# Kernel tuning notes

Hardware: AMD Instinct MI355X
Metric: run time of the kernel (lower is better)

The kernel has to match this reference:

```python
import jax, jax.numpy as jnp
import numpy as np

B, S, D, H = 2, 2048, 768, 12
HD = D // H  # head_dim = 64


def setup_inputs() -> dict:
    key = jax.random.key(0)
    ks = jax.random.split(key, 9)
    s = 1.0 / np.sqrt(D)
    return {
        "x": jax.random.normal(ks[0], (B, S, D), dtype=jnp.float32),
        "Wq": jax.random.normal(ks[1], (D, D), dtype=jnp.float32) * s,
        "bq": jnp.zeros((D,), dtype=jnp.float32),
        "Wk": jax.random.normal(ks[2], (D, D), dtype=jnp.float32) * s,
        "bk": jnp.zeros((D,), dtype=jnp.float32),
        "Wv": jax.random.normal(ks[3], (D, D), dtype=jnp.float32) * s,
        "bv": jnp.zeros((D,), dtype=jnp.float32),
        "Wo": jax.random.normal(ks[4], (D, D), dtype=jnp.float32) * s,
        "bo": jnpp if False else jnp.zeros((D,), dtype=jnp.float32),
    }


def reference(x, Wq, bq, Wk, bk, Wv, bv, Wo, bo):
    b, s, d = x.shape
    # projections, split heads: [b, h, s, hd]
    def proj(W, bias):
        y = x @ W + bias
        return y.reshape(b, s, H, HD).transpose(0, 2, 1, 3)

    q = proj(Wq, bq)
    k = proj(Wk, bk)
    v = proj(Wv, bv)

    scale = 1.0 / jnp.sqrt(jnp.float32(HD))
    scores = jnp.einsum("bhqd,bhkd->bhqk", q, k) * scale
    causal = jnp.tril(jnp.ones((s, s), dtype=bool))  # True where allowed
    scores = jnp.where(causal, scores, -jnp.inf)
    attn = jax.nn.softmax(scores, axis=-1)
    ctx = jnp.einsum("bhqk,bhkd->bhqd", attn, v)
    ctx = ctx.transpose(0, 2, 1, 3).reshape(b, s, d)
    return ctx @ Wo + bo
```

## Files before the change

### kernel.cpp

```cpp
#include <hip/hip_runtime.h>
#include <stdint.h>

typedef unsigned short u16;
typedef __attribute__((ext_vector_type(8))) short s16x8;
typedef __attribute__((ext_vector_type(4))) float f32x4;
typedef __attribute__((ext_vector_type(16))) float f32x16;

#define MFMA_BF16(a, b, c) __builtin_amdgcn_mfma_f32_16x16x32_bf16((a), (b), (c), 0, 0, 0)
#define MFMA32(a, b, c) __builtin_amdgcn_mfma_f32_32x32x16_bf16((a), (b), (c), 0, 0, 0)

typedef const __attribute__((address_space(1))) uint32_t* gas1_t;
typedef __attribute__((address_space(3))) uint32_t* las3_t;
#define GLDS16(dst, src) __builtin_amdgcn_global_load_lds((gas1_t)(src), (las3_t)(dst), 16, 0, 0)

static __device__ __forceinline__ u16 f2bf(float f) {
    uint32_t u = __float_as_uint(f);
    u = (u + 0x7fffu + ((u >> 16) & 1u)) >> 16;
    return (u16)u;
}
static __device__ __forceinline__ uint32_t pk2bf(float a, float b) {
    return (uint32_t)f2bf(a) | ((uint32_t)f2bf(b) << 16);
}
static __device__ __forceinline__ float bf2f(u16 h) {
    return __uint_as_float(((uint32_t)h) << 16);
}

__global__ __launch_bounds__(256) void k_prep(const float* __restrict__ x, u16* __restrict__ xb,
                                              const float* __restrict__ w0, const float* __restrict__ w1,
                                              const float* __restrict__ w2, const float* __restrict__ w3,
                                              u16* __restrict__ t0, u16* __restrict__ t1,
                                              u16* __restrict__ t2, u16* __restrict__ t3) {
    __shared__ float tile[32][33];
    const int bid = blockIdx.x, t = threadIdx.x;
    if (bid < 1536) {
        const int i = (bid * 256 + t) * 8;
        f32x4 a = *(const f32x4*)(x + i);
        f32x4 b = *(const f32x4*)(x + i + 4);
        s16x8 r;
        r[0] = (short)f2bf(a[0]); r[1] = (short)f2bf(a[1]);
        r[2] = (short)f2bf(a[2]); r[3] = (short)f2bf(a[3]);
        r[4] = (short)f2bf(b[0]); r[5] = (short)f2bf(b[1]);
        r[6] = (short)f2bf(b[2]); r[7] = (short)f2bf(b[3]);
        *(s16x8*)(xb + i) = r;
        return;
    }
    const int u = bid - 1536;
    const int z = u / 576, r2 = u - z * 576;
    const float* W; u16* T;
    switch (z) {
        case 0:  W = w0; T = t0; break;
        case 1:  W = w1; T = t1; break;
        case 2:  W = w2; T = t2; break;
        default: W = w3; T = t3; break;
    }
    const int n0 = (r2 % 24) * 32, k0 = (r2 / 24) * 32;
    const int tx = t & 31, ty = t >> 5;
#pragma unroll
    for (int i = 0; i < 4; ++i)
        tile[ty + 8 * i][tx] = W[(size_t)(k0 + ty + 8 * i) * 768 + n0 + tx];
    __syncthreads();
#pragma unroll
    for (int i = 0; i < 4; ++i)
        T[(size_t)(n0 + ty + 8 * i) * 768 + k0 + tx] = f2bf(tile[tx][ty + 8 * i]);
}

__global__ __launch_bounds__(256) void k_gemm_qkv(
        const u16* __restrict__ A,
        const u16* __restrict__ btq, const u16* __restrict__ btk, const u16* __restrict__ btv,
        const float* __restrict__ bq, const float* __restrict__ bk, const float* __restrict__ bv,
        u16* __restrict__ outq, u16* __restrict__ outk, u16* __restrict__ outv) {
    __shared__ u16 lA[2][128 * 64];
    __shared__ u16 lB[2][64 * 64];
    const int cid = blockIdx.x;
    const int swz = (cid & 7) * 144 + (cid >> 3);
    const int sx = swz % 36, by = swz / 36;
    const int sel = sx / 12, nb = sx - sel * 12;
    const u16* Bt; const float* bias;
    if (sel == 0)      { Bt = btq; bias = bq; }
    else if (sel == 1) { Bt = btk; bias = bk; }
    else               { Bt = btv; bias = bv; }
    const int t = threadIdx.x, lane = t & 63, w = t >> 6;
    const int wr = w >> 1, wc = w & 1;
    const int c = lane & 15, g = lane >> 4;
    const int m0 = by * 128, n0 = nb * 64;
    f32x4 acc[4][2] = {};
    const int lr = lane >> 3, lg = lane & 7;
    const int swz8 = 8 * (lg ^ lr);
    const u16* gA = A  + (size_t)(m0 + w * 8 + lr) * 768 + swz8;
    const u16* gB = Bt + (size_t)(n0 + w * 8 + lr) * 768 + swz8;
#define STG_QKV(bb, kb)                                                        \
    {                                                                          \
        _Pragma("unroll")                                                      \
        for (int j = 0; j < 4; ++j)                                            \
            GLDS16(&lA[bb][j * 2048 + w * 512], gA + (size_t)j * 32 * 768 + (kb)); \
        _Pragma("unroll")                                                      \
        for (int j = 0; j < 2; ++j)                                            \
            GLDS16(&lB[bb][j * 2048 + w * 512], gB + (size_t)j * 32 * 768 + (kb)); \
    }
    STG_QKV(0, 0);
    for (int ki = 0; ki < 12; ++ki) {
        const int cur = ki & 1;
        if (ki + 1 < 12) {
            STG_QKV(cur ^ 1, (ki + 1) * 64);
            asm volatile("s_waitcnt vmcnt(6)" ::: "memory");
        } else {
            asm volatile("s_waitcnt vmcnt(0)" ::: "memory");
        }
        __builtin_amdgcn_sched_barrier(0);
        __builtin_amdgcn_s_barrier();
#pragma unroll
        for (int kh = 0; kh < 2; ++kh) {
            s16x8 af[4], bfr[2];
            const int gg = kh * 4 + g;
#pragma unroll
            for (int i = 0; i < 4; ++i) {
                const int ra = wr * 64 + i * 16 + c;
                af[i] = *(const s16x8*)&lA[cur][ra * 64 + 8 * (gg ^ (ra & 7))];
            }
#pragma unroll
            for (int j = 0; j < 2; ++j) {
                const int rb = wc * 32 + j * 16 + c;
                bfr[j] = *(const s16x8*)&lB[cur][rb * 64 + 8 * (gg ^ (rb & 7))];
            }
#pragma unroll
            for (int i = 0; i < 4; ++i)
#pragma unroll
                for (int j = 0; j < 2; ++j)
                    acc[i][j] = MFMA_BF16(af[i], bfr[j], acc[i][j]);
        }
        __builtin_amdgcn_s_barrier();
    }
#undef STG_QKV
    const float C2 = 0.18033688011112042f;
    const int h = nb;
    if (sel < 2) {
        u16* outp = (sel == 0) ? outq : outk;
        const float osc = (sel == 0) ? C2 : 1.0f;
#pragma unroll
        for (int i = 0; i < 4; ++i)
#pragma unroll
            for (int j = 0; j < 2; ++j) {
                const int hd = wc * 32 + j * 16 + c;
                const float bvv = bias[n0 + hd];
#pragma unroll
                for (int rr = 0; rr < 4; ++rr) {
                    const int m = m0 + wr * 64 + i * 16 + g * 4 + rr;
                    const int b = m >> 11, s = m & 2047;
                    outp[(((size_t)(b * 12 + h) * 2048 + s) << 6) + hd] =
                        f2bf((acc[i][j][rr] + bvv) * osc);
                }
            }
    } else {
#pragma unroll
        for (int i = 0; i < 4; ++i)
#pragma unroll
            for (int j = 0; j < 2; ++j) {
                const int hd = wc * 32 + j * 16 + c;
                const float bvv = bias[n0 + hd];
                const int m = m0 + wr * 64 + i * 16 + g * 4;
                const int b = m >> 11, s = m & 2047;
                uint64_t pk = (uint64_t)pk2bf(acc[i][j][0] + bvv, acc[i][j][1] + bvv) |
                              ((uint64_t)pk2bf(acc[i][j][2] + bvv, acc[i][j][3] + bvv) << 32);
                *(uint64_t*)&outv[((size_t)(b * 12 + h) * 64 + hd) * 2048 + s] = pk;
            }
    }
}

__global__ __launch_bounds__(256) void k_gemm_out(const u16* __restrict__ A,
                                                  const u16* __restrict__ Bt,
                                                  const float* __restrict__ bias,
                                                  float* __restrict__ out) {
    __shared__ u16 lA[2][64 * 64];
    __shared__ u16 lB[2][64 * 64];
    const int cid = blockIdx.x;
    const int swz = (cid & 7) * 96 + (cid >> 3);
    const int bx = swz % 12, by = swz / 12;
    const int t = threadIdx.x;
    const int lane = t & 63, w = t >> 6;
    const int wr = w >> 1, wc = w & 1;
    const int c = lane & 15, g = lane >> 4;
    const int m0 = by * 64, n0 = bx * 64;
    f32x4 acc[2][2] = {};
    const int lr = lane >> 3, lq = lane & 7;
    const int sq = (lq ^ lr) * 8;
    const u16* gA0 = A  + (size_t)(m0 + w * 16 + lr) * 768 + sq;
    const u16* gA1 = gA0 + 8 * 768;
    const u16* gB0 = Bt + (size_t)(n0 + w * 16 + lr) * 768 + sq;
    const u16* gB1 = gB0 + 8 * 768;
#define STG_OUT(bb, kb)                                                        \
    {                                                                          \
        GLDS16(&lA[bb][w * 1024], gA0 + (kb));                                 \
        GLDS16(&lA[bb][w * 1024 + 512], gA1 + (kb));                           \
        GLDS16(&lB[bb][w * 1024], gB0 + (kb));                                 \
        GLDS16(&lB[bb][w * 1024 + 512], gB1 + (kb));                           \
    }
    STG_OUT(0, 0);
    for (int ki = 0; ki < 12; ++ki) {
        const int cur = ki & 1;
        if (ki + 1 < 12) {
            STG_OUT(cur ^ 1, (ki + 1) * 64);
            asm volatile("s_waitcnt vmcnt(4)" ::: "memory");
        } else {
            asm volatile("s_waitcnt vmcnt(0)" ::: "memory");
        }
        __builtin_amdgcn_sched_barrier(0);
        __builtin_amdgcn_s_barrier();
#pragma unroll
        for (int st = 0; st < 2; ++st) {
            s16x8 af[2], bf[2];
            const int col = st * 32 + g * 8;
#pragma unroll
            for (int i = 0; i < 2; ++i) {
                int ra = wr * 32 + i * 16 + c;
                af[i] = *(const s16x8*)&lA[cur][ra * 64 + (col ^ ((ra & 7) << 3))];
                int rb = wc * 32 + i * 16 + c;
                bf[i] = *(const s16x8*)&lB[cur][rb * 64 + (col ^ ((rb & 7) << 3))];
            }
#pragma unroll
            for (int i = 0; i < 2; ++i)
#pragma unroll
                for (int j = 0; j < 2; ++j)
                    acc[i][j] = MFMA_BF16(af[i], bf[j], acc[i][j]);
        }
        __builtin_amdgcn_s_barrier();
    }
#undef STG_OUT
#pragma unroll
    for (int i = 0; i < 2; ++i)
#pragma unroll
        for (int j = 0; j < 2; ++j) {
            const int n = n0 + wc * 32 + j * 16 + c;
            const float bvv = bias[n];
#pragma unroll
            for (int rr = 0; rr < 4; ++rr) {
                const int m = m0 + wr * 32 + i * 16 + g * 4 + rr;
                out[(size_t)m * 768 + n] = acc[i][j][rr] + bvv;
            }
        }
}

__device__ static const signed char SLOT_QT[40] = {
    15,15,15,15, 14,14,14,14, 13,13,13,13, 12,12,12,12,
    11,11,11, 10,10,10, 9,9,9, 8,8,8, 7,7, 6,6, 5,5, 4,4, 3, 2, 1, 0};
__device__ static const signed char SLOT_SEG[40] = {
    0,1,2,3, 0,1,2,3, 0,1,2,3, 0,1,2,3,
    0,1,2, 0,1,2, 0,1,2, 0,1,2, 0,1, 0,1, 0,1, 0,1, 0, 0, 0, 0};

__global__ __launch_bounds__(256) void k_attn(const u16* __restrict__ qw,
                                              const u16* __restrict__ kw,
                                              const u16* __restrict__ vt,
                                              u16* __restrict__ ctxb,
                                              u16* __restrict__ pctx,
                                              float* __restrict__ pm,
                                              float* __restrict__ ps) {
    const int bid = blockIdx.x;
    const int slot = bid / 24, j24 = bid - slot * 24;
    const int bh = (j24 & 7) * 3 + (j24 >> 3);
    const int qt = SLOT_QT[slot], seg = SLOT_SEG[slot];
    const int nseg = (2 * (qt + 1) + 7) >> 3;
    const int ch0 = seg * 8;
    const int rem = 2 * (qt + 1) - ch0;
    const int nch = rem < 8 ? rem : 8;
    const int t = threadIdx.x, lane = t & 63, w = t >> 6;
    const int l31 = lane & 31, hi = lane >> 5;
    const int q0w = qt * 128 + w * 32;
    const u16* qp = qw + (size_t)bh * 2048 * 64;
    const u16* kp = kw + (size_t)bh * 2048 * 64;
    const u16* vp = vt + (size_t)bh * 64 * 2048;
    s16x8 qf[4];
#pragma unroll
    for (int dk = 0; dk < 4; ++dk)
        qf[dk] = *(const s16x8*)&qp[(size_t)(q0w + l31) * 64 + dk * 16 + hi * 8];
    const int lastq = q0w + 31;
    const int lastch = (lastq >> 6) + 1 - ch0;
    const int mynch = nch < lastch ? nch : lastch;
    f32x16 ct[2] = {};
    float m2 = -1e30f, ssum = 0.0f;
    for (int ci = 0; ci < mynch; ++ci) {
        const int Kc = (ch0 + ci) * 64;
        const u16* kr0 = kp + (size_t)(Kc + l31) * 64;
        const u16* kr1 = kp + (size_t)(Kc + 32 + l31) * 64;
        f32x16 st[2] = {};
#pragma unroll
        for (int dk = 0; dk < 4; ++dk) {
            const int gr = dk * 2 + hi;
            s16x8 kf0 = *(const s16x8*)&kr0[gr * 8];
            s16x8 kf1 = *(const s16x8*)&kr1[gr * 8];
            st[0] = MFMA32(kf0, qf[dk], st[0]);
            st[1] = MFMA32(kf1, qf[dk], st[1]);
        }
        const int qg = q0w + l31;
        float tv[32];
        if (Kc + 63 <= q0w) {
#pragma unroll
            for (int j = 0; j < 16; ++j) { tv[j] = st[0][j]; tv[16 + j] = st[1][j]; }
        } else {
            const int kb = Kc + 4 * hi;
#pragma unroll
            for (int j = 0; j < 16; ++j) {
                const int kloc = (j & 3) + 8 * (j >> 2);
                tv[j]      = (kb + kloc      <= qg) ? st[0][j] : -1e30f;
                tv[16 + j] = (kb + kloc + 32 <= qg) ? st[1][j] : -1e30f;
            }
        }
        float x16[16], x8[8], x4[4];
#pragma unroll
        for (int j = 0; j < 16; ++j) x16[j] = fmaxf(tv[j], tv[j + 16]);
#pragma unroll
        for (int j = 0; j < 8; ++j) x8[j] = fmaxf(x16[j], x16[j + 8]);
#pragma unroll
        for (int j = 0; j < 4; ++j) x4[j] = fmaxf(x8[j], x8[j + 4]);
        const float mt = fmaxf(fmaxf(x4[0], x4[1]), fmaxf(x4[2], x4[3]));
        if (!__all(mt <= m2 + 8.0f)) {
            float mq = fmaxf(mt, __shfl_xor(mt, 32));
            const float mnew = fmaxf(m2, mq);
            const float fac = __builtin_amdgcn_exp2f(m2 - mnew);
            ssum *= fac;
#pragma unroll
            for (int j = 0; j < 16; ++j) { ct[0][j] *= fac; ct[1][j] *= fac; }
            m2 = mnew;
        }
        float p[32];
#pragma unroll
        for (int j = 0; j < 32; ++j) p[j] = __builtin_amdgcn_exp2f(tv[j] - m2);
        float y16[16], y8[8], y4[4];
#pragma unroll
        for (int j = 0; j < 16; ++j) y16[j] = p[j] + p[j + 16];
#pragma unroll
        for (int j = 0; j < 8; ++j) y8[j] = y16[j] + y16[j + 8];
#pragma unroll
        for (int j = 0; j < 4; ++j) y4[j] = y8[j] + y8[j + 4];
        ssum += (y4[0] + y4[1]) + (y4[2] + y4[3]);
#pragma unroll
        for (int kt = 0; kt < 2; ++kt) {
            uint32_t pcv[8];
#pragma unroll
            for (int x = 0; x < 8; ++x) {
                const int j = kt * 16 + 4 * (x >> 1) + 2 * (x & 1);
                asm volatile("v_cvt_pk_bf16_f32 %0, %1, %2"
                             : "=v"(pcv[x]) : "v"(p[j]), "v"(p[j + 1]));
            }
#pragma unroll
            for (int kl = 0; kl < 2; ++kl) {
                uint32_t a0 = pcv[4 * kl],     b0 = pcv[4 * kl + 2];
                uint32_t a1 = pcv[4 * kl + 1], b1 = pcv[4 * kl + 3];
                asm volatile("v_permlane32_swap_b32 %0, %1" : "+v"(a0), "+v"(b0));
                asm volatile("v_permlane32_swap_b32 %0, %1" : "+v"(a1), "+v"(b1));
                union { uint32_t u[4]; s16x8 v; } pf;
                pf.u[0] = a0; pf.u[1] = a1; pf.u[2] = b0; pf.u[3] = b1;
                const int ko = Kc + (kt * 2 + kl) * 16 + hi * 8;
                s16x8 vf0 = *(const s16x8*)&vp[(size_t)l31 * 2048 + ko];
                s16x8 vf1 = *(const s16x8*)&vp[(size_t)(32 + l31) * 2048 + ko];
                ct[0] = MFMA32(vf0, pf.v, ct[0]);
                ct[1] = MFMA32(vf1, pf.v, ct[1]);
            }
        }
    }
    if (nseg == 1) {
        ssum += __shfl_xor(ssum, 32);
        const float inv = 1.0f / ssum;
        const int b = bh / 12, h = bh - b * 12;
        const size_t base = (size_t)(b * 2048 + q0w + l31) * 768 + h * 64;
#pragma unroll
        for (int ht = 0; ht < 2; ++ht)
#pragma unroll
            for (int a = 0; a < 4; ++a) {
                const int hd = ht * 32 + 8 * a + 4 * hi;
                uint64_t pk = (uint64_t)pk2bf(ct[ht][4 * a] * inv, ct[ht][4 * a + 1] * inv) |
                              ((uint64_t)pk2bf(ct[ht][4 * a + 2] * inv, ct[ht][4 * a + 3] * inv) << 32);
                *(uint64_t*)&ctxb[base + hd] = pk;
            }
    } else {
        const float srow = ssum + __shfl_xor(ssum, 32);
        const int ti = (bh * 16 + qt) * 4 + seg;
        const int row = w * 32 + l31;
        u16* pp = &pctx[(size_t)ti * 8192 + row * 64];
#pragma unroll
        for (int ht = 0; ht < 2; ++ht)
#pragma unroll
            for (int a = 0; a < 4; ++a) {
                const int hd = ht * 32 + 8 * a + 4 * hi;
                uint64_t pk = (uint64_t)pk2bf(ct[ht][4 * a], ct[ht][4 * a + 1]) |
                              ((uint64_t)pk2bf(ct[ht][4 * a + 2], ct[ht][4 * a + 3]) << 32);
                *(uint64_t*)&pp[hd] = pk;
            }
        if (hi == 0) {
            pm[ti * 128 + row] = m2;
            ps[ti * 128 + row] = srow;
        }
    }
}

__global__ __launch_bounds__(256) void k_attn_combine(const u16* __restrict__ pctx,
                                                      const float* __restrict__ pm,
                                                      const float* __restrict__ ps,
                                                      u16* __restrict__ ctxb) {
    const int bh = blockIdx.x, qt = blockIdx.y + 4;
    const int nseg = (2 * (qt + 1) + 7) >> 3;
    const int tb = (bh * 16 + qt) * 4;
    const int b = bh / 12, h = bh - b * 12;
#pragma unroll
    for (int it = 0; it < 2; ++it) {
        const int u = threadIdx.x + it * 256;
        const int row = u >> 2, h0 = (u & 3) * 16;
        float mv[4], sv[4];
#pragma unroll
        for (int s = 0; s < 4; ++s) {
            mv[s] = (s < nseg) ? pm[(tb + s) * 128 + row] : -1e30f;
            sv[s] = (s < nseg) ? ps[(tb + s) * 128 + row] : 0.0f;
        }
        const float mstar = fmaxf(fmaxf(mv[0], mv[1]), fmaxf(mv[2], mv[3]));
        float wv[4], S = 0.0f;
#pragma unroll
        for (int s = 0; s < 4; ++s) {
            wv[s] = __builtin_amdgcn_exp2f(mv[s] - mstar);
            S += wv[s] * sv[s];
        }
        float acc[16] = {};
#pragma unroll
        for (int s = 0; s < 4; ++s) {
            if (s < nseg) {
                const u16* pp = &pctx[(size_t)(tb + s) * 8192 + row * 64 + h0];
                const float wgt = wv[s];
#pragma unroll
                for (int e = 0; e < 2; ++e) {
                    s16x8 v = *(const s16x8*)(pp + e * 8);
#pragma unroll
                    for (int x = 0; x < 8; ++x)
                        acc[e * 8 + x] += wgt * bf2f((u16)v[x]);
                }
            }
        }
        const float inv = 1.0f / S;
        u16* op = &ctxb[(size_t)(b * 2048 + qt * 128 + row) * 768 + h * 64 + h0];
        s16x8 o0, o1;
#pragma unroll
        for (int x = 0; x < 8; ++x) {
            o0[x] = (short)f2bf(acc[x] * inv);
            o1[x] = (short)f2bf(acc[8 + x] * inv);
        }
        *(s16x8*)op = o0;
        *(s16x8*)(op + 8) = o1;
    }
}

extern "C" void kernel_launch(void* const* d_in, const int* in_sizes, int n_in,
                              void* d_out, int out_size, void* d_ws, size_t ws_size,
                              hipStream_t stream) {
    (void)in_sizes; (void)n_in; (void)out_size; (void)ws_size;
    const float* x  = (const float*)d_in[0];
    const float* Wq = (const float*)d_in[1];
    const float* bq = (const float*)d_in[2];
    const float* Wk = (const float*)d_in[3];
    const float* bk = (const float*)d_in[4];
    const float* Wv = (const float*)d_in[5];
    const float* bv = (const float*)d_in[6];
    const float* Wo = (const float*)d_in[7];
    const float* bo = (const float*)d_in[8];
    char* ws = (char*)d_ws;
    u16* xb   = (u16*)(ws);
    u16* wqt  = (u16*)(ws + 6291456);
    u16* wkt  = (u16*)(ws + 7471104);
    u16* wvt  = (u16*)(ws + 8650752);
    u16* wot  = (u16*)(ws + 9830400);
    u16* qwv  = (u16*)(ws + 11010048);
    u16* kwv  = (u16*)(ws + 17301504);
    u16* vtw  = (u16*)(ws + 23592960);
    u16* ctx  = (u16*)(ws + 29884416);
    u16* pctx = (u16*)(ws + 36175872);
    float* pm = (float*)(ws + 61341696);
    float* psu= (float*)(ws + 62128128);
    float* out = (float*)d_out;

    k_prep<<<3840, 256, 0, stream>>>(x, xb, Wq, Wk, Wv, Wo, wqt, wkt, wvt, wot);
    k_gemm_qkv<<<1152, 256, 0, stream>>>(xb, wqt, wkt, wvt, bq, bk, bv, qwv, kwv, vtw);
    k_attn<<<960, 256, 0, stream>>>(qwv, kwv, vtw, ctx, pctx, pm, psu);
    k_attn_combine<<<dim3(24, 12), 256, 0, stream>>>(pctx, pm, psu, ctx);
    k_gemm_out<<<768, 256, 0, stream>>>(ctx, wot, bo, out);
}
```

Baseline: 187.7 us.

## Stage K tiles via async global-to-LDS double buffer with 32-key chunks

The attention kernel now processes 32-key chunks instead of 64. K tiles are staged per wave into a swizzled, double-buffered LDS region using async global_load_lds, with explicit vmcnt waits so the next chunk's load overlaps compute on the current one. V fragments are loaded before the score MFMAs to hide their latency. The finer chunks also trim causal work on the diagonal. In exchange the loop runs twice as many iterations with more per-iteration overhead, and it relies on hand-counted vmcnt values that must stay in sync with the other outstanding loads.

Result: faster. 172.0 us (-8.3%).

```diff
diff --git a/kernel.cpp b/kernel.cpp
--- a/kernel.cpp
+++ b/kernel.cpp
@@ -253,14 +253,13 @@
                                               u16* __restrict__ pctx,
                                               float* __restrict__ pm,
                                               float* __restrict__ ps) {
+    __shared__ u16 lK[4][2][32 * 64];
     const int bid = blockIdx.x;
     const int slot = bid / 24, j24 = bid - slot * 24;
     const int bh = (j24 & 7) * 3 + (j24 >> 3);
     const int qt = SLOT_QT[slot], seg = SLOT_SEG[slot];
     const int nseg = (2 * (qt + 1) + 7) >> 3;
-    const int ch0 = seg * 8;
-    const int rem = 2 * (qt + 1) - ch0;
-    const int nch = rem < 8 ? rem : 8;
+    const int ch0 = seg * 16;
     const int t = threadIdx.x, lane = t & 63, w = t >> 6;
     const int l31 = lane & 31, hi = lane >> 5;
     const int q0w = qt * 128 + w * 32;
@@ -272,42 +271,63 @@
     for (int dk = 0; dk < 4; ++dk)
         qf[dk] = *(const s16x8*)&qp[(size_t)(q0w + l31) * 64 + dk * 16 + hi * 8];
     const int lastq = q0w + 31;
-    const int lastch = (lastq >> 6) + 1 - ch0;
-    const int mynch = nch < lastch ? nch : lastch;
+    const int avail = (lastq >> 5) + 1 - ch0;
+    const int mynch = avail < 16 ? avail : 16;
+    const int lr = lane >> 3, lg = lane & 7;
+    const u16* kpb = kp + (size_t)lr * 64 + 8 * (lg ^ (lr & 7));
+    u16* lKw = &lK[w][0][0];
+    int koff[4];
+#pragma unroll
+    for (int dk = 0; dk < 4; ++dk)
+        koff[dk] = l31 * 64 + 8 * ((dk * 2 + hi) ^ (l31 & 7));
     f32x16 ct[2] = {};
     float m2 = -1e30f, ssum = 0.0f;
+#define STAGE32(bf, ch)                                                        \
+    {                                                                          \
+        const u16* ks_ = kpb + (size_t)(ch) * 2048;                            \
+        GLDS16(lKw + (bf) * 2048, ks_);                                        \
+        GLDS16(lKw + (bf) * 2048 + 512, ks_ + 512);                            \
+        GLDS16(lKw + (bf) * 2048 + 1024, ks_ + 1024);                          \
+        GLDS16(lKw + (bf) * 2048 + 1536, ks_ + 1536);                          \
+    }
+    STAGE32(0, ch0);
     for (int ci = 0; ci < mynch; ++ci) {
-        const int Kc = (ch0 + ci) * 64;
-        const u16* kr0 = kp + (size_t)(Kc + l31) * 64;
-        const u16* kr1 = kp + (size_t)(Kc + 32 + l31) * 64;
-        f32x16 st[2] = {};
+        const int bf = ci & 1, Kc = (ch0 + ci) * 32;
+        s16x8 vf0[2], vf1[2];
+#pragma unroll
+        for (int kl = 0; kl < 2; ++kl) {
+            const int ko = Kc + kl * 16 + hi * 8;
+            vf0[kl] = *(const s16x8*)&vp[(size_t)l31 * 2048 + ko];
+            vf1[kl] = *(const s16x8*)&vp[(size_t)(32 + l31) * 2048 + ko];
+        }
+        if (ci + 1 < mynch) {
+            STAGE32(bf ^ 1, ch0 + ci + 1);
+            asm volatile("s_waitcnt vmcnt(8)" ::: "memory");
+        } else {
+            asm volatile("s_waitcnt vmcnt(4)" ::: "memory");
+        }
+        f32x16 st = {};
 #pragma unroll
         for (int dk = 0; dk < 4; ++dk) {
-            const int gr = dk * 2 + hi;
-            s16x8 kf0 = *(const s16x8*)&kr0[gr * 8];
-            s16x8 kf1 = *(const s16x8*)&kr1[gr * 8];
-            st[0] = MFMA32(kf0, qf[dk], st[0]);
-            st[1] = MFMA32(kf1, qf[dk], st[1]);
+            s16x8 kf = *(const s16x8*)&lKw[bf * 2048 + koff[dk]];
+            st = MFMA32(kf, qf[dk], st);
         }
         const int qg = q0w + l31;
-        float tv[32];
-        if (Kc + 63 <= q0w) {
-#pragma unroll
-            for (int j = 0; j < 16; ++j) { tv[j] = st[0][j]; tv[16 + j] = st[1][j]; }
+        float tv[16];
+        if (Kc + 31 <= q0w) {
+#pragma unroll
+            for (int j = 0; j < 16; ++j) tv[j] = st[j];
         } else {
             const int kb = Kc + 4 * hi;
 #pragma unroll
             for (int j = 0; j < 16; ++j) {
                 const int kloc = (j & 3) + 8 * (j >> 2);
-                tv[j]      = (kb + kloc      <= qg) ? st[0][j] : -1e30f;
-                tv[16 + j] = (kb + kloc + 32 <= qg) ? st[1][j] : -1e30f;
-            }
-        }
-        float x16[16], x8[8], x4[4];
-#pragma unroll
-        for (int j = 0; j < 16; ++j) x16[j] = fmaxf(tv[j], tv[j + 16]);
-#pragma unroll
-        for (int j = 0; j < 8; ++j) x8[j] = fmaxf(x16[j], x16[j + 8]);
+                tv[j] = (kb + kloc <= qg) ? st[j] : -1e30f;
+            }
+        }
+        float x8[8], x4[4];
+#pragma unroll
+        for (int j = 0; j < 8; ++j) x8[j] = fmaxf(tv[j], tv[j + 8]);
 #pragma unroll
         for (int j = 0; j < 4; ++j) x4[j] = fmaxf(x8[j], x8[j + 4]);
         const float mt = fmaxf(fmaxf(x4[0], x4[1]), fmaxf(x4[2], x4[3]));
@@ -320,40 +340,32 @@
             for (int j = 0; j < 16; ++j) { ct[0][j] *= fac; ct[1][j] *= fac; }
             m2 = mnew;
         }
-        float p[32];
-#pragma unroll
-        for (int j = 0; j < 32; ++j) p[j] = __builtin_amdgcn_exp2f(tv[j] - m2);
-        float y16[16], y8[8], y4[4];
-#pragma unroll
-        for (int j = 0; j < 16; ++j) y16[j] = p[j] + p[j + 16];
-#pragma unroll
-        for (int j = 0; j < 8; ++j) y8[j] = y16[j] + y16[j + 8];
+        float p[16];
+#pragma unroll
+        for (int j = 0; j < 16; ++j) p[j] = __builtin_amdgcn_exp2f(tv[j] - m2);
+        float y8[8], y4[4];
+#pragma unroll
+        for (int j = 0; j < 8; ++j) y8[j] = p[j] + p[j + 8];
 #pragma unroll
         for (int j = 0; j < 4; ++j) y4[j] = y8[j] + y8[j + 4];
         ssum += (y4[0] + y4[1]) + (y4[2] + y4[3]);
-#pragma unroll
-        for (int kt = 0; kt < 2; ++kt) {
-            uint32_t pcv[8];
-#pragma unroll
-            for (int x = 0; x < 8; ++x) {
-                const int j = kt * 16 + 4 * (x >> 1) + 2 * (x & 1);
-                asm volatile("v_cvt_pk_bf16_f32 %0, %1, %2"
-                             : "=v"(pcv[x]) : "v"(p[j]), "v"(p[j + 1]));
-            }
-#pragma unroll
-            for (int kl = 0; kl < 2; ++kl) {
-                uint32_t a0 = pcv[4 * kl],     b0 = pcv[4 * kl + 2];
-                uint32_t a1 = pcv[4 * kl + 1], b1 = pcv[4 * kl + 3];
-                asm volatile("v_permlane32_swap_b32 %0, %1" : "+v"(a0), "+v"(b0));
-                asm volatile("v_permlane32_swap_b32 %0, %1" : "+v"(a1), "+v"(b1));
-                union { uint32_t u[4]; s16x8 v; } pf;
-                pf.u[0] = a0; pf.u[1] = a1; pf.u[2] = b0; pf.u[3] = b1;
-                const int ko = Kc + (kt * 2 + kl) * 16 + hi * 8;
-                s16x8 vf0 = *(const s16x8*)&vp[(size_t)l31 * 2048 + ko];
-                s16x8 vf1 = *(const s16x8*)&vp[(size_t)(32 + l31) * 2048 + ko];
-                ct[0] = MFMA32(vf0, pf.v, ct[0]);
-                ct[1] = MFMA32(vf1, pf.v, ct[1]);
-            }
+        uint32_t pcv[8];
+#pragma unroll
+        for (int x = 0; x < 8; ++x) {
+            const int j = 4 * (x >> 1) + 2 * (x & 1);
+            asm volatile("v_cvt_pk_bf16_f32 %0, %1, %2"
+                         : "=v"(pcv[x]) : "v"(p[j]), "v"(p[j + 1]));
+        }
+#pragma unroll
+        for (int kl = 0; kl < 2; ++kl) {
+            uint32_t a0 = pcv[4 * kl],     b0 = pcv[4 * kl + 2];
+            uint32_t a1 = pcv[4 * kl + 1], b1 = pcv[4 * kl + 3];
+            asm volatile("v_permlane32_swap_b32 %0, %1" : "+v"(a0), "+v"(b0));
+            asm volatile("v_permlane32_swap_b32 %0, %1" : "+v"(a1), "+v"(b1));
+            union { uint32_t u[4]; s16x8 v; } pf;
+            pf.u[0] = a0; pf.u[1] = a1; pf.u[2] = b0; pf.u[3] = b1;
+            ct[0] = MFMA32(vf0[kl], pf.v, ct[0]);
+            ct[1] = MFMA32(vf1[kl], pf.v, ct[1]);
         }
     }
     if (nseg == 1) {
@@ -389,6 +401,7 @@
             ps[ti * 128 + row] = srow;
         }
     }
+#undef STAGE32
 }
 
 __global__ __launch_bounds__(256) void k_attn_combine(const u16* __restrict__ pctx,
```
